# Optimization experiments

Measured on AMD Instinct MI355X. Metric: run time of the kernel, lower is better.

The kernel has to match this reference:

```python
import jax, jax.numpy as jnp
import numpy as np
from jax import lax

IMG = 1280
VAR0, VAR1 = 0.1, 0.2          # SSD decode variances
CONF_T = 0.7                    # confidence threshold
NMS_T = 0.4                     # IoU threshold
K = 1000                        # fixed NMS candidate budget (jit-friendly)
MIN_SIZES = [[16, 32], [64, 128], [256, 512]]
STEPS = [8, 16, 32]


def make_priors():
    """Vectorized priorbox: [cx, cy, w, h] normalized to [0,1]. N = 67200."""
    out = []
    for ms, s in zip(MIN_SIZES, STEPS):
        f = IMG // s
        ii, jj = np.meshgrid(np.arange(f), np.arange(f), indexing='ij')
        cx = (jj + 0.5) * s / IMG
        cy = (ii + 0.5) * s / IMG
        per_m = [np.stack([cx, cy, np.full_like(cx, m / IMG, dtype=np.float64),
                           np.full_like(cx, m / IMG, dtype=np.float64)], axis=-1)
                 for m in ms]
        a = np.stack(per_m, axis=2)  # [f, f, n_min_sizes, 4] -> matches (i, j, min_size) loop order
        out.append(a.reshape(-1, 4))
    return np.concatenate(out, axis=0).astype(np.float32)


def setup_inputs() -> dict:
    key = jax.random.key(0)
    k1, k2, k3 = jax.random.split(key, 3)
    N = 67200
    loc = jax.random.normal(k1, (1, N, 4), dtype=jnp.float32)
    conf = jax.random.normal(k2, (1, N, 2), dtype=jnp.float32)
    land = jax.random.normal(k3, (1, N, 10), dtype=jnp.float32)
    priors = jnp.asarray(make_priors())
    return {"loc": loc, "conf": conf, "land": land, "priors": priors}


def _decode_boxes(loc, priors):
    # center-form decode then convert to corner form (x1,y1,x2,y2)
    xy = priors[:, :2] + loc[:, :2] * VAR0 * priors[:, 2:]
    wh = priors[:, 2:] * jnp.exp(loc[:, 2:] * VAR1)
    x1y1 = xy - wh * 0.5
    return jnp.concatenate([x1y1, x1y1 + wh], axis=-1)


def _decode_landm(land, priors):
    l = land.reshape(-1, 5, 2)  # 5 landmark points
    pts = priors[:, None, :2] + l * VAR0 * priors[:, None, 2:]
    return pts.reshape(-1, 10)


def _pairwise_iou(b):
    # b: [K, 4] corner-form
    area = (b[:, 2] - b[:, 0]) * (b[:, 3] - b[:, 1])
    lt = jnp.maximum(b[:, None, :2], b[None, :, :2])
    rb = jnp.minimum(b[:, None, 2:], b[None, :, 2:])
    wh = jnp.clip(rb - lt, 0.0)
    inter = wh[..., 0] * wh[..., 1]
    return inter / (area[:, None] + area[None, :] - inter + 1e-12)


def reference(loc, conf, land, priors):
    scores_all = jax.nn.softmax(conf[0], axis=-1)[:, 1]          # [N]
    boxes_all = _decode_boxes(loc[0], priors) * IMG              # [N, 4]
    landms_all = _decode_landm(land[0], priors) * IMG            # [N, 10]

    # threshold (torch.where) + fixed-size top-K selection for jit
    masked = jnp.where(scores_all > CONF_T, scores_all, -jnp.inf)
    top_s, idx = lax.top_k(masked, K)                            # sorted descending
    b = boxes_all[idx]
    lm = landms_all[idx]
    s = scores_all[idx]
    valid = top_s > CONF_T                                       # slots that passed threshold

    # greedy NMS over score-sorted candidates
    iou = _pairwise_iou(b)                                       # [K, K]
    ar = jnp.arange(K)

    def body(i, keep):
        sup = (iou[i] > NMS_T) & (ar > i) & keep[i]
        return keep & ~sup

    keep = lax.fori_loop(0, K, body, valid)

    boxes_out = jnp.where(keep[:, None], b, 0.0)
    scores_out = jnp.where(keep, s, 0.0)
    landms_out = jnp.where(keep[:, None], lm, 0.0)
    return boxes_out, scores_out, landms_out
```

## Files before the change

kernel.cpp:

```cpp
#include <hip/hip_runtime.h>
#include <stdint.h>

#define N_ANCH 67200
#define KCAP   1000
#define CONF_THR 0.7f
#define NMS_THR  0.4f

#define BUCK_BASE 0x3F333333u
#define BUCK_SHIFT 10
#define NBUCK 5120
#define CAPG 4096

#define MID_BLKS 32
#define RNK_BLKS 4

#define OFF_CTR   0
#define OFF_HIST  64
#define OFF_FILL  20544
#define OFF_LIST  41024
#define OFF_GKEYS 578624
#define OFF_SCORE 611392
#define OFF_BOX   615488
#define OFF_LM    631872
#define OFF_SUP   672832

__device__ inline unsigned long long shfl_xor_u64(unsigned long long v, int m) {
    unsigned int lo = (unsigned int)__shfl_xor((int)(v & 0xffffffffull), m, 64);
    unsigned int hi = (unsigned int)__shfl_xor((int)(v >> 32), m, 64);
    return ((unsigned long long)hi << 32) | lo;
}

__device__ inline int bucket_of(unsigned int sb) {
    return min((int)((sb - BUCK_BASE) >> BUCK_SHIFT), NBUCK - 1);
}

__device__ inline void findcut_and_scan(int* sufx, int* swsum, int* sB,
                                        int tid, int lane, int wv) {
    if (tid < 64) {
        int acc = 0, B = 0;
        bool found = false;
        for (int t = 0; t < NBUCK / 64 && !found; ++t) {
            int base = NBUCK - 64 * (t + 1);
            int c = sufx[base + lane];
            int ssum = c;
#pragma unroll
            for (int off = 1; off < 64; off <<= 1)
                ssum += __shfl_xor(ssum, off, 64);
            if (acc + ssum >= KCAP) {
                for (int l = 63; l >= 0; --l) {
                    int cl = (int)__builtin_amdgcn_readlane((unsigned int)c, l);
                    if (acc + cl >= KCAP) { B = base + l; found = true; break; }
                    acc += cl;
                }
            } else {
                acc += ssum;
            }
        }
        if (lane == 0) *sB = found ? B : 0;
    }
    __syncthreads();
    int c[5];
#pragma unroll
    for (int k = 0; k < 5; ++k)
        c[k] = sufx[NBUCK - 1 - (tid * 5 + k)];
    int tsum = c[0] + c[1] + c[2] + c[3] + c[4];
    int inc = tsum;
#pragma unroll
    for (int off = 1; off < 64; off <<= 1) {
        int n = __shfl_up(inc, off, 64);
        if (lane >= off) inc += n;
    }
    if (lane == 63) swsum[wv] = inc;
    __syncthreads();
    if (tid < 16) {
        int v = swsum[tid];
        int s = v;
#pragma unroll
        for (int off = 1; off < 16; off <<= 1) {
            int n = __shfl_up(s, off, 64);
            if (tid >= off) s += n;
        }
        swsum[tid] = s - v;
    }
    __syncthreads();
    int run = swsum[wv] + inc - tsum;
#pragma unroll
    for (int k = 0; k < 5; ++k) {
        sufx[NBUCK - 1 - (tid * 5 + k)] = run;
        run += c[k];
    }
    __syncthreads();
}

__global__ __launch_bounds__(1024) void k_zero(int* __restrict__ ctr,
                                               int* __restrict__ hist,
                                               int* __restrict__ gfill) {
    int tid = threadIdx.x;
    if (tid < 16) ctr[tid] = 0;
    for (int t = tid; t < NBUCK; t += 1024) { hist[t] = 0; gfill[t] = 0; }
}

__global__ __launch_bounds__(256) void k_front(const float* __restrict__ conf,
                                               unsigned long long* __restrict__ list,
                                               int* __restrict__ hist,
                                               int* __restrict__ ctr) {
    int t = blockIdx.x * 256 + threadIdx.x;
    int lane = threadIdx.x & 63;
    int a0 = t * 2;
    bool p0 = false, p1 = false;
    unsigned long long k0 = 0ull, k1 = 0ull;
    if (a0 < N_ANCH) {
        float4 c = reinterpret_cast<const float4*>(conf)[t];
        {
            float mx = fmaxf(c.x, c.y);
            float e0 = expf(c.x - mx), e1 = expf(c.y - mx);
            float s = e1 / (e0 + e1);
            if (s > CONF_THR) {
                p0 = true;
                k0 = ((unsigned long long)__float_as_uint(s) << 32)
                   | (unsigned int)(0xFFFFFFFFu - (unsigned int)a0);
            }
        }
        {
            float mx = fmaxf(c.z, c.w);
            float e0 = expf(c.z - mx), e1 = expf(c.w - mx);
            float s = e1 / (e0 + e1);
            if (s > CONF_THR) {
                p1 = true;
                k1 = ((unsigned long long)__float_as_uint(s) << 32)
                   | (unsigned int)(0xFFFFFFFFu - (unsigned int)(a0 + 1));
            }
        }
    }
    unsigned long long m0 = __ballot(p0);
    unsigned long long m1 = __ballot(p1);
    int n0 = (int)__popcll(m0), n1 = (int)__popcll(m1);
    int base = 0;
    if ((n0 + n1) > 0) {
        if (lane == 0) base = atomicAdd(&ctr[0], n0 + n1);
        base = __shfl(base, 0, 64);
        unsigned long long below = (1ull << lane) - 1ull;
        if (p0) {
            list[base + (int)__popcll(m0 & below)] = k0;
            atomicAdd(&hist[bucket_of((unsigned int)(k0 >> 32))], 1);
        }
        if (p1) {
            list[base + n0 + (int)__popcll(m1 & below)] = k1;
            atomicAdd(&hist[bucket_of((unsigned int)(k1 >> 32))], 1);
        }
    }
}

__global__ __launch_bounds__(1024) void k_mid(
        const unsigned long long* __restrict__ list,
        const int* __restrict__ hist,
        int* __restrict__ gfill,
        unsigned long long* __restrict__ gkeys,
        const int* __restrict__ ctr) {
    __shared__ int sufx[NBUCK];
    __shared__ int swsum[16];
    __shared__ int sB;
    int tid = threadIdx.x, lane = tid & 63, wv = tid >> 6;
    for (int t = tid; t < NBUCK; t += 1024) sufx[t] = hist[t];
    __syncthreads();
    findcut_and_scan(sufx, swsum, &sB, tid, lane, wv);
    int B = sB;
    int M = min(ctr[0], N_ANCH);
    for (int p = blockIdx.x * 1024 + tid; p < M; p += MID_BLKS * 1024) {
        unsigned long long k = list[p];
        int b = bucket_of((unsigned int)(k >> 32));
        if (b >= B) {
            int off = atomicAdd(&gfill[b], 1);
            int slot = sufx[b] + off;
            if (slot < CAPG) gkeys[slot] = k;
        }
    }
}

__global__ __launch_bounds__(1024) void k_rankdec(
        const unsigned long long* __restrict__ gkeys,
        const int* __restrict__ hist,
        const int* __restrict__ gfill,
        const int* __restrict__ ctr,
        const float* __restrict__ loc,
        const float* __restrict__ land,
        const float* __restrict__ priors,
        float* __restrict__ sel_score,
        float* __restrict__ sel_box,
        float* __restrict__ sel_lm) {
#pragma clang fp contract(off)
    __shared__ int sufx[NBUCK];
    __shared__ int swsum[16];
    __shared__ int sB;
    int tid = threadIdx.x, lane = tid & 63, wv = tid >> 6;
    for (int t = tid; t < NBUCK; t += 1024) sufx[t] = hist[t];
    __syncthreads();
    findcut_and_scan(sufx, swsum, &sB, tid, lane, wv);
    int B = sB;
    int M = min(ctr[0], N_ANCH);
    int S = min((B > 0) ? sufx[B - 1] : M, CAPG);

    for (int s = blockIdx.x * 1024 + tid; s < S; s += RNK_BLKS * 1024) {
        unsigned long long key = gkeys[s];
        unsigned int sb = (unsigned int)(key >> 32);
        int b = bucket_of(sb);
        int seg0 = sufx[b];
        int segn = gfill[b];
        int within = 0;
        for (int t = 0; t < segn && seg0 + t < CAPG; ++t)
            within += (gkeys[seg0 + t] > key) ? 1 : 0;
        int r = seg0 + within;
        if (r < KCAP) {
            unsigned int a = 0xFFFFFFFFu - (unsigned int)(key & 0xFFFFFFFFull);
            sel_score[r] = __uint_as_float(sb);
            float pcx = priors[a*4+0], pcy = priors[a*4+1];
            float pw  = priors[a*4+2], ph  = priors[a*4+3];
            float l0 = loc[a*4+0], l1 = loc[a*4+1], l2 = loc[a*4+2], l3 = loc[a*4+3];
            float cx = pcx + (l0 * 0.1f) * pw;
            float cy = pcy + (l1 * 0.1f) * ph;
            float w  = pw * expf(l2 * 0.2f);
            float h2 = ph * expf(l3 * 0.2f);
            float x1 = cx - w * 0.5f;
            float y1 = cy - h2 * 0.5f;
            sel_box[r*4+0] = x1 * 1280.0f;
            sel_box[r*4+1] = y1 * 1280.0f;
            sel_box[r*4+2] = (x1 + w) * 1280.0f;
            sel_box[r*4+3] = (y1 + h2) * 1280.0f;
#pragma unroll
            for (int q = 0; q < 5; ++q) {
                float lx = land[a*10 + 2*q + 0];
                float ly = land[a*10 + 2*q + 1];
                sel_lm[r*10 + 2*q + 0] = (pcx + (lx * 0.1f) * pw) * 1280.0f;
                sel_lm[r*10 + 2*q + 1] = (pcy + (ly * 0.1f) * ph) * 1280.0f;
            }
        }
    }
}

__global__ __launch_bounds__(256) void k_sup(const float* __restrict__ sel_box,
                                             const int* __restrict__ ctr,
                                             unsigned long long* __restrict__ sup) {
#pragma clang fp contract(off)
    int lane = threadIdx.x & 63, wv = threadIdx.x >> 6;
    int i = blockIdx.x * 4 + wv;
    int V = min(ctr[0], KCAP);
    bool irow = (i < V);
    float ax1 = 0.f, ay1 = 0.f, ax2 = 0.f, ay2 = 0.f, aarea = 0.f;
    if (irow) {
        ax1 = sel_box[i*4+0]; ay1 = sel_box[i*4+1];
        ax2 = sel_box[i*4+2]; ay2 = sel_box[i*4+3];
        aarea = (ax2 - ax1) * (ay2 - ay1);
    }
    for (int g = 0; g < 16; ++g) {
        int j = g * 64 + lane;
        bool pred = false;
        if (irow && j < V && j > i) {
            float4 b = reinterpret_cast<const float4*>(sel_box)[j];
            float barea = (b.z - b.x) * (b.w - b.y);
            float ltx = fmaxf(ax1, b.x), lty = fmaxf(ay1, b.y);
            float rbx = fminf(ax2, b.z), rby = fminf(ay2, b.w);
            float wx = fmaxf(rbx - ltx, 0.0f);
            float wy = fmaxf(rby - lty, 0.0f);
            float inter = wx * wy;
            float iou = inter / (aarea + barea - inter + 1e-12f);
            pred = iou > NMS_THR;
        }
        unsigned long long mask = __ballot(pred);
        if (lane == 0) sup[i*16 + g] = mask;
    }
}

__global__ __launch_bounds__(1024) void k_nms_scan(
        const unsigned long long* __restrict__ sup,
        const int* __restrict__ ctr,
        const float* __restrict__ sel_score,
        const float* __restrict__ sel_box,
        const float* __restrict__ sel_lm,
        float* __restrict__ out) {
    __shared__ unsigned long long sup_r[1024][16];
    __shared__ unsigned long long mshare[16];
    __shared__ unsigned long long keep_final[16];
    int tid = threadIdx.x;
    int wave = tid >> 6, lane = tid & 63;
    int V = min(ctr[0], KCAP);

    for (int idx = tid; idx < KCAP * 16; idx += 1024) {
        int r = idx >> 4, w = idx & 15;
        sup_r[r][w ^ (r & 15)] = sup[idx];
    }
    if (tid < 24 * 16) {
        int r = 1000 + (tid >> 4), w = tid & 15;
        sup_r[r][w ^ (r & 15)] = 0ull;
    }
    unsigned long long kw;
    {
        int lo = wave * 64;
        kw = (V >= lo + 64) ? ~0ull : (V <= lo ? 0ull : ((1ull << (V - lo)) - 1ull));
    }
    __syncthreads();

    for (int c = 0; c < 16; ++c) {
        if (wave == c) {
            unsigned long long drow = sup_r[c*64 + lane][c ^ (lane & 15)];
            unsigned int dlo = (unsigned int)drow;
            unsigned int dhi = (unsigned int)(drow >> 32);
            unsigned long long nz = __ballot(drow != 0ull);
            unsigned long long m = kw;
            unsigned long long todo = m & nz;
            while (todo) {
                int i = (int)__builtin_ctzll(todo);
                i = __builtin_amdgcn_readfirstlane(i);
                unsigned long long di =
                    (((unsigned long long)(unsigned int)__builtin_amdgcn_readlane(dhi, i)) << 32)
                  |  (unsigned long long)(unsigned int)__builtin_amdgcn_readlane(dlo, i);
                m &= ~di;
                todo &= ~di;
                todo &= todo - 1ull;
            }
            kw = m;
            if (lane == 0) mshare[c] = m;
        }
        __syncthreads();
        if (wave > c) {
            unsigned long long m = mshare[c];
            unsigned long long contrib = ((m >> lane) & 1ull)
                ? sup_r[c*64 + lane][wave ^ (lane & 15)] : 0ull;
            if (__ballot(contrib != 0ull) != 0ull) {
#pragma unroll
                for (int off = 1; off < 64; off <<= 1)
                    contrib |= shfl_xor_u64(contrib, off);
                kw &= ~contrib;
            }
        }
    }
    if (lane == 0) keep_final[wave] = kw;
    __syncthreads();

    for (int s = tid; s < KCAP; s += 1024) {
        bool kept = ((keep_final[s >> 6] >> (s & 63)) & 1ull) != 0ull;
        float4 b = make_float4(0.f, 0.f, 0.f, 0.f);
        float sc = 0.f;
        if (kept) {
            b  = reinterpret_cast<const float4*>(sel_box)[s];
            sc = sel_score[s];
        }
        reinterpret_cast<float4*>(out)[s] = b;
        out[4000 + s] = sc;
#pragma unroll
        for (int q = 0; q < 10; ++q)
            out[5000 + s*10 + q] = kept ? sel_lm[s*10 + q] : 0.f;
    }
}

extern "C" void kernel_launch(void* const* d_in, const int* in_sizes, int n_in,
                              void* d_out, int out_size, void* d_ws, size_t ws_size,
                              hipStream_t stream) {
    const float* loc    = (const float*)d_in[0];
    const float* conf   = (const float*)d_in[1];
    const float* land   = (const float*)d_in[2];
    const float* priors = (const float*)d_in[3];
    float* out = (float*)d_out;
    char* ws = (char*)d_ws;

    int* ctr                     = (int*)(ws + OFF_CTR);
    int* hist                    = (int*)(ws + OFF_HIST);
    int* gfill                   = (int*)(ws + OFF_FILL);
    unsigned long long* list     = (unsigned long long*)(ws + OFF_LIST);
    unsigned long long* gkeys    = (unsigned long long*)(ws + OFF_GKEYS);
    float* sel_score             = (float*)(ws + OFF_SCORE);
    float* sel_box               = (float*)(ws + OFF_BOX);
    float* sel_lm                = (float*)(ws + OFF_LM);
    unsigned long long* sup      = (unsigned long long*)(ws + OFF_SUP);

    int nfb = (N_ANCH / 2 + 255) / 256;
    k_zero<<<1, 1024, 0, stream>>>(ctr, hist, gfill);
    k_front<<<nfb, 256, 0, stream>>>(conf, list, hist, ctr);
    k_mid<<<MID_BLKS, 1024, 0, stream>>>(list, hist, gfill, gkeys, ctr);
    k_rankdec<<<RNK_BLKS, 1024, 0, stream>>>(gkeys, hist, gfill, ctr,
                                             loc, land, priors,
                                             sel_score, sel_box, sel_lm);
    k_sup<<<KCAP / 4, 256, 0, stream>>>(sel_box, ctr, sup);
    k_nms_scan<<<1, 1024, 0, stream>>>(sup, ctr, sel_score, sel_box, sel_lm, out);
}
```

Baseline: 64.96 us.

## Fuse mid/rank and sup/scan kernels via last-block-done atomic counters

Merges the bucket-scatter kernel with the rank/decode kernel, and the suppression-matrix kernel with the NMS scan kernel. Each pair uses a global atomic counter so that only the last finishing block continues into the serial second phase. This removes two kernel launches and their inter-kernel gaps. In exchange, the rank/decode phase now runs in a single block instead of four, and every suppression block reserves the large shared buffer needed only by the scan.

```diff
diff --git a/kernel.cpp b/kernel.cpp
--- a/kernel.cpp
+++ b/kernel.cpp
@@ -12,7 +12,7 @@
 #define CAPG 4096
 
 #define MID_BLKS 32
-#define RNK_BLKS 4
+#define SUP_BLKS 63
 
 #define OFF_CTR   0
 #define OFF_HIST  64
@@ -151,37 +151,12 @@
     }
 }
 
-__global__ __launch_bounds__(1024) void k_mid(
+__global__ __launch_bounds__(1024) void k_midrank(
         const unsigned long long* __restrict__ list,
         const int* __restrict__ hist,
         int* __restrict__ gfill,
         unsigned long long* __restrict__ gkeys,
-        const int* __restrict__ ctr) {
-    __shared__ int sufx[NBUCK];
-    __shared__ int swsum[16];
-    __shared__ int sB;
-    int tid = threadIdx.x, lane = tid & 63, wv = tid >> 6;
-    for (int t = tid; t < NBUCK; t += 1024) sufx[t] = hist[t];
-    __syncthreads();
-    findcut_and_scan(sufx, swsum, &sB, tid, lane, wv);
-    int B = sB;
-    int M = min(ctr[0], N_ANCH);
-    for (int p = blockIdx.x * 1024 + tid; p < M; p += MID_BLKS * 1024) {
-        unsigned long long k = list[p];
-        int b = bucket_of((unsigned int)(k >> 32));
-        if (b >= B) {
-            int off = atomicAdd(&gfill[b], 1);
-            int slot = sufx[b] + off;
-            if (slot < CAPG) gkeys[slot] = k;
-        }
-    }
-}
-
-__global__ __launch_bounds__(1024) void k_rankdec(
-        const unsigned long long* __restrict__ gkeys,
-        const int* __restrict__ hist,
-        const int* __restrict__ gfill,
-        const int* __restrict__ ctr,
+        int* __restrict__ ctr,
         const float* __restrict__ loc,
         const float* __restrict__ land,
         const float* __restrict__ priors,
@@ -192,15 +167,36 @@
     __shared__ int sufx[NBUCK];
     __shared__ int swsum[16];
     __shared__ int sB;
+    __shared__ int slast;
     int tid = threadIdx.x, lane = tid & 63, wv = tid >> 6;
     for (int t = tid; t < NBUCK; t += 1024) sufx[t] = hist[t];
     __syncthreads();
     findcut_and_scan(sufx, swsum, &sB, tid, lane, wv);
     int B = sB;
     int M = min(ctr[0], N_ANCH);
+
+    for (int p = blockIdx.x * 1024 + tid; p < M; p += MID_BLKS * 1024) {
+        unsigned long long k = list[p];
+        int b = bucket_of((unsigned int)(k >> 32));
+        if (b >= B) {
+            int off = atomicAdd(&gfill[b], 1);
+            int slot = sufx[b] + off;
+            if (slot < CAPG) gkeys[slot] = k;
+        }
+    }
+    __syncthreads();
+    if (tid == 0) {
+        __threadfence();
+        int old = atomicAdd(&ctr[1], 1);
+        slast = (old == MID_BLKS - 1);
+    }
+    __syncthreads();
+    if (!slast) return;
+    if (tid == 0) __threadfence();
+    __syncthreads();
+
     int S = min((B > 0) ? sufx[B - 1] : M, CAPG);
-
-    for (int s = blockIdx.x * 1024 + tid; s < S; s += RNK_BLKS * 1024) {
+    for (int s = tid; s < S; s += 1024) {
         unsigned long long key = gkeys[s];
         unsigned int sb = (unsigned int)(key >> 32);
         int b = bucket_of(sb);
@@ -237,52 +233,61 @@
     }
 }
 
-__global__ __launch_bounds__(256) void k_sup(const float* __restrict__ sel_box,
-                                             const int* __restrict__ ctr,
-                                             unsigned long long* __restrict__ sup) {
+__global__ __launch_bounds__(1024) void k_supscan(
+        const float* __restrict__ sel_box,
+        const float* __restrict__ sel_score,
+        const float* __restrict__ sel_lm,
+        int* __restrict__ ctr,
+        unsigned long long* __restrict__ sup,
+        float* __restrict__ out) {
 #pragma clang fp contract(off)
-    int lane = threadIdx.x & 63, wv = threadIdx.x >> 6;
-    int i = blockIdx.x * 4 + wv;
-    int V = min(ctr[0], KCAP);
-    bool irow = (i < V);
-    float ax1 = 0.f, ay1 = 0.f, ax2 = 0.f, ay2 = 0.f, aarea = 0.f;
-    if (irow) {
-        ax1 = sel_box[i*4+0]; ay1 = sel_box[i*4+1];
-        ax2 = sel_box[i*4+2]; ay2 = sel_box[i*4+3];
-        aarea = (ax2 - ax1) * (ay2 - ay1);
-    }
-    for (int g = 0; g < 16; ++g) {
-        int j = g * 64 + lane;
-        bool pred = false;
-        if (irow && j < V && j > i) {
-            float4 b = reinterpret_cast<const float4*>(sel_box)[j];
-            float barea = (b.z - b.x) * (b.w - b.y);
-            float ltx = fmaxf(ax1, b.x), lty = fmaxf(ay1, b.y);
-            float rbx = fminf(ax2, b.z), rby = fminf(ay2, b.w);
-            float wx = fmaxf(rbx - ltx, 0.0f);
-            float wy = fmaxf(rby - lty, 0.0f);
-            float inter = wx * wy;
-            float iou = inter / (aarea + barea - inter + 1e-12f);
-            pred = iou > NMS_THR;
-        }
-        unsigned long long mask = __ballot(pred);
-        if (lane == 0) sup[i*16 + g] = mask;
-    }
-}
-
-__global__ __launch_bounds__(1024) void k_nms_scan(
-        const unsigned long long* __restrict__ sup,
-        const int* __restrict__ ctr,
-        const float* __restrict__ sel_score,
-        const float* __restrict__ sel_box,
-        const float* __restrict__ sel_lm,
-        float* __restrict__ out) {
     __shared__ unsigned long long sup_r[1024][16];
     __shared__ unsigned long long mshare[16];
     __shared__ unsigned long long keep_final[16];
+    __shared__ int slast;
     int tid = threadIdx.x;
     int wave = tid >> 6, lane = tid & 63;
     int V = min(ctr[0], KCAP);
+
+    {
+        int i = blockIdx.x * 16 + wave;
+        if (i < KCAP) {
+            bool irow = (i < V);
+            float ax1 = 0.f, ay1 = 0.f, ax2 = 0.f, ay2 = 0.f, aarea = 0.f;
+            if (irow) {
+                ax1 = sel_box[i*4+0]; ay1 = sel_box[i*4+1];
+                ax2 = sel_box[i*4+2]; ay2 = sel_box[i*4+3];
+                aarea = (ax2 - ax1) * (ay2 - ay1);
+            }
+            for (int g = 0; g < 16; ++g) {
+                int j = g * 64 + lane;
+                bool pred = false;
+                if (irow && j < V && j > i) {
+                    float4 b = reinterpret_cast<const float4*>(sel_box)[j];
+                    float barea = (b.z - b.x) * (b.w - b.y);
+                    float ltx = fmaxf(ax1, b.x), lty = fmaxf(ay1, b.y);
+                    float rbx = fminf(ax2, b.z), rby = fminf(ay2, b.w);
+                    float wx = fmaxf(rbx - ltx, 0.0f);
+                    float wy = fmaxf(rby - lty, 0.0f);
+                    float inter = wx * wy;
+                    float iou = inter / (aarea + barea - inter + 1e-12f);
+                    pred = iou > NMS_THR;
+                }
+                unsigned long long mask = __ballot(pred);
+                if (lane == 0) sup[i*16 + g] = mask;
+            }
+        }
+    }
+    __syncthreads();
+    if (tid == 0) {
+        __threadfence();
+        int old = atomicAdd(&ctr[2], 1);
+        slast = (old == SUP_BLKS - 1);
+    }
+    __syncthreads();
+    if (!slast) return;
+    if (tid == 0) __threadfence();
+    __syncthreads();
 
     for (int idx = tid; idx < KCAP * 16; idx += 1024) {
         int r = idx >> 4, w = idx & 15;
@@ -375,10 +380,9 @@
     int nfb = (N_ANCH / 2 + 255) / 256;
     k_zero<<<1, 1024, 0, stream>>>(ctr, hist, gfill);
     k_front<<<nfb, 256, 0, stream>>>(conf, list, hist, ctr);
-    k_mid<<<MID_BLKS, 1024, 0, stream>>>(list, hist, gfill, gkeys, ctr);
-    k_rankdec<<<RNK_BLKS, 1024, 0, stream>>>(gkeys, hist, gfill, ctr,
+    k_midrank<<<MID_BLKS, 1024, 0, stream>>>(list, hist, gfill, gkeys, ctr,
                                              loc, land, priors,
                                              sel_score, sel_box, sel_lm);
-    k_sup<<<KCAP / 4, 256, 0, stream>>>(sel_box, ctr, sup);
-    k_nms_scan<<<1, 1024, 0, stream>>>(sup, ctr, sel_score, sel_box, sel_lm, out);
-}
+    k_supscan<<<SUP_BLKS, 1024, 0, stream>>>(sel_box, sel_score, sel_lm, ctr,
+                                             sup, out);
+}
```

Measured after the change: 60.30 us. -7.2%, faster.
